# Performance work log

Hardware: AMD Instinct MI355X
Metric: run time of the kernel (lower is better)

## Reference

```python
import jax, jax.numpy as jnp
import numpy as np

HS, FF, NH = 1024, 4096, 16
HD = HS // NH
EPS = 1e-5

def _ln(x, g, b):
    m = jnp.mean(x, axis=-1, keepdims=True)
    v = jnp.mean((x - m) ** 2, axis=-1, keepdims=True)
    return (x - m) * jax.lax.rsqrt(v + EPS) * g + b

def setup_inputs() -> dict:
    key = jax.random.key(0)
    ks = jax.random.split(key, 12)
    s = 1.0 / np.sqrt(HS)
    si = 1.0 / np.sqrt(FF)
    d = {
        "hidden_states": jax.random.normal(ks[0], (2, 2048, HS), dtype=jnp.float32),
        "attention_mask": jnp.zeros((2, 1, 1, 2048), dtype=jnp.float32),
        "Wq": jax.random.uniform(ks[1], (HS, HS), minval=-s, maxval=s),
        "bq": jnp.zeros((HS,), jnp.float32),
        "Wk": jax.random.uniform(ks[2], (HS, HS), minval=-s, maxval=s),
        "bk": jnp.zeros((HS,), jnp.float32),
        "Wv": jax.random.uniform(ks[3], (HS, HS), minval=-s, maxval=s),
        "bv": jnp.zeros((HS,), jnp.float32),
        "Wo": jax.random.uniform(ks[4], (HS, HS), minval=-s, maxval=s),
        "bo": jnp.zeros((HS,), jnp.float32),
        "W1": jax.random.uniform(ks[5], (HS, FF), minval=-s, maxval=s),
        "b1": jnp.zeros((FF,), jnp.float32),
        "W2": jax.random.uniform(ks[6], (FF, HS), minval=-si, maxval=si),
        "b2": jnp.zeros((HS,), jnp.float32),
        "ln1_g": jnp.ones((HS,), jnp.float32),
        "ln1_b": jnp.zeros((HS,), jnp.float32),
        "ln2_g": jnp.ones((HS,), jnp.float32),
        "ln2_b": jnp.zeros((HS,), jnp.float32),
    }
    return d

def reference(hidden_states, attention_mask, Wq, bq, Wk, bk, Wv, bv, Wo, bo,
              W1, b1, W2, b2, ln1_g, ln1_b, ln2_g, ln2_b):
    bs, S, _ = hidden_states.shape
    x = hidden_states
    # self-attention (dropout is identity in eval)
    q = (x @ Wq + bq).reshape(bs, S, NH, HD).transpose(0, 2, 1, 3)
    k = (x @ Wk + bk).reshape(bs, S, NH, HD).transpose(0, 2, 1, 3)
    v = (x @ Wv + bv).reshape(bs, S, NH, HD).transpose(0, 2, 1, 3)
    scores = jnp.einsum("bhqd,bhkd->bhqk", q, k) / np.sqrt(HD) + attention_mask
    probs = jax.nn.softmax(scores, axis=-1)
    attn = jnp.einsum("bhqk,bhkd->bhqd", probs, v)
    attn = attn.transpose(0, 2, 1, 3).reshape(bs, S, HS)
    mha = attn @ Wo + bo
    h = _ln(x + mha, ln1_g, ln1_b)
    # FFN
    ff = jax.nn.relu(h @ W1 + b1) @ W2 + b2
    return _ln(h + ff, ln2_g, ln2_b)
```

## Files before the change

kernel.cpp:

```cpp
#include <hip/hip_runtime.h>
#include <hip/hip_bf16.h>

#define HS   1024
#define FF   4096
#define NH   16
#define HD   64
#define SEQ  2048
#define BSZ  2
#define MROWS (BSZ * SEQ)
#define EPS  1e-5f
#define QKV_STRIDE (3 * HS)

typedef float f32x4  __attribute__((ext_vector_type(4)));
typedef short bf16x8 __attribute__((ext_vector_type(8)));

#if __has_builtin(__builtin_amdgcn_exp2f)
#define EXP2(x) __builtin_amdgcn_exp2f(x)
#else
#define EXP2(x) exp2f(x)
#endif

__device__ __forceinline__ unsigned short f2bf(float x) {
  unsigned int u = __float_as_uint(x);
  u += 0x7fffu + ((u >> 16) & 1u);
  return (unsigned short)(u >> 16);
}

__device__ __forceinline__ float bf2f(unsigned short u) {
  return __uint_as_float((unsigned int)u << 16);
}

__device__ __forceinline__ unsigned int pkbf(float a, float b) {
  union { __hip_bfloat162 h; unsigned int u; } x;
  x.h = __float22bfloat162_rn(float2{a, b});
  return x.u;
}

__device__ __forceinline__ void async16(const ushort* g, ushort* lds) {
  __builtin_amdgcn_global_load_lds(
      (const __attribute__((address_space(1))) unsigned int*)g,
      (__attribute__((address_space(3))) unsigned int*)lds, 16, 0, 0);
}

template <int TBM, int TBN, bool RELU, bool OUT_BF16, bool PARTIAL>
__global__ __launch_bounds__(256) void gemm_bf16_kernel(
    const ushort* __restrict__ A, const ushort* __restrict__ Bt,
    const float* __restrict__ bias, void* __restrict__ Cout,
    int M, int N, int K, int kLen, size_t zstride)
{
  constexpr int MI = TBM / 32;
  constexpr int NJ = TBN / 32;
  __shared__ ushort As[TBM * 64];
  __shared__ ushort Bs[TBN * 64];

  const int tid = threadIdx.x;
  const int wv = tid >> 6, ln = tid & 63;

  const unsigned nxy = gridDim.x * gridDim.y;
  unsigned id = blockIdx.y * gridDim.x + blockIdx.x;
  id = (id & 7) * (nxy >> 3) + (id >> 3);
  const int bn = id % gridDim.x, bm = id / gridDim.x;

  const int lr = ln & 15;
  const int lg = ln >> 4;
  const int mrow_base = (wv >> 1) * (TBM / 2);
  const int ncol_base = (wv & 1) * (TBN / 2);

  f32x4 acc[MI][NJ];
#pragma unroll
  for (int i = 0; i < MI; ++i)
#pragma unroll
    for (int j = 0; j < NJ; ++j) acc[i][j] = (f32x4){0.f, 0.f, 0.f, 0.f};

  const int rr = ln >> 3, cc = ln & 7;
  const int kBeg = blockIdx.z * kLen, kEnd = kBeg + kLen;

  for (int k0 = kBeg; k0 < kEnd; k0 += 64) {
    __syncthreads();
#pragma unroll
    for (int t = 0; t < TBM / 32; ++t) {
      const int R = wv * (TBM / 4) + t * 8 + rr;
      const int c = cc ^ (R & 7);
      async16(A + (size_t)(bm * TBM + R) * K + k0 + c * 8,
              &As[(size_t)(wv * (TBM / 4) + t * 8) * 64]);
    }
#pragma unroll
    for (int t = 0; t < TBN / 32; ++t) {
      const int R = wv * (TBN / 4) + t * 8 + rr;
      const int c = cc ^ (R & 7);
      async16(Bt + (size_t)(bn * TBN + R) * K + k0 + c * 8,
              &Bs[(size_t)(wv * (TBN / 4) + t * 8) * 64]);
    }
    __syncthreads();

#pragma unroll
    for (int s = 0; s < 2; ++s) {
      bf16x8 a[MI], b[NJ];
#pragma unroll
      for (int i = 0; i < MI; ++i) {
        const int m = mrow_base + i * 16 + lr;
        a[i] = *(const bf16x8*)&As[(size_t)m * 64 + (((s * 4 + lg) ^ (m & 7)) * 8)];
      }
#pragma unroll
      for (int j = 0; j < NJ; ++j) {
        const int n = ncol_base + j * 16 + lr;
        b[j] = *(const bf16x8*)&Bs[(size_t)n * 64 + (((s * 4 + lg) ^ (n & 7)) * 8)];
      }
#pragma unroll
      for (int i = 0; i < MI; ++i)
#pragma unroll
        for (int j = 0; j < NJ; ++j)
          acc[i][j] = __builtin_amdgcn_mfma_f32_16x16x32_bf16(a[i], b[j], acc[i][j], 0, 0, 0);
    }
  }

  const int gm0 = bm * TBM + mrow_base;
  const int gn0 = bn * TBN + ncol_base;

  if (PARTIAL) {
    float* Cp = (float*)Cout + (size_t)blockIdx.z * zstride;
#pragma unroll
    for (int i = 0; i < MI; ++i)
#pragma unroll
      for (int r = 0; r < 4; ++r) {
        const size_t row = (size_t)(gm0 + i * 16 + lg * 4 + r);
#pragma unroll
        for (int j = 0; j < NJ; ++j)
          Cp[row * N + gn0 + j * 16 + lr] = acc[i][j][r];
      }
  } else {
    float bs4[NJ];
#pragma unroll
    for (int j = 0; j < NJ; ++j) bs4[j] = bias[gn0 + j * 16 + lr];
    float* Cf = (float*)Cout;
    ushort* Cb = (ushort*)Cout;
#pragma unroll
    for (int i = 0; i < MI; ++i) {
#pragma unroll
      for (int r = 0; r < 4; ++r) {
        const size_t row = (size_t)(gm0 + i * 16 + lg * 4 + r);
#pragma unroll
        for (int j = 0; j < NJ; ++j) {
          float val = acc[i][j][r] + bs4[j];
          if (RELU) val = fmaxf(val, 0.f);
          const size_t idx = row * N + gn0 + j * 16 + lr;
          if (OUT_BF16) Cb[idx] = f2bf(val);
          else          Cf[idx] = val;
        }
      }
    }
  }
}

__device__ __forceinline__ void transpose_tile(
    const float* __restrict__ W, ushort* __restrict__ Wt,
    int K, int N, int n0, int k0, int tid, ushort (*T)[72])
{
#pragma unroll
  for (int t = 0; t < 4; ++t) {
    const int r = t * 16 + (tid >> 4);
    const int c = (tid & 15) * 4;
    const float4 w = *(const float4*)&W[(size_t)(k0 + r) * N + n0 + c];
    T[c + 0][r] = f2bf(w.x); T[c + 1][r] = f2bf(w.y);
    T[c + 2][r] = f2bf(w.z); T[c + 3][r] = f2bf(w.w);
  }
  __syncthreads();
#pragma unroll
  for (int t = 0; t < 4; ++t) {
    const int n = t * 16 + (tid >> 4);
    const int kc = (tid & 15) * 4;
    ushort4 o;
    o.x = T[n][kc]; o.y = T[n][kc + 1]; o.z = T[n][kc + 2]; o.w = T[n][kc + 3];
    *(ushort4*)&Wt[(size_t)(n0 + n) * K + k0 + kc] = o;
  }
}

__global__ __launch_bounds__(256) void prep_kernel(
    const float* __restrict__ Wq, const float* __restrict__ Wk,
    const float* __restrict__ Wv, const float* __restrict__ Wo,
    const float* __restrict__ W1, const float* __restrict__ W2,
    const float* __restrict__ bq, const float* __restrict__ bk,
    const float* __restrict__ bv, const float* __restrict__ x,
    const float* __restrict__ mask,
    ushort* __restrict__ Wqkvt, ushort* __restrict__ Wot,
    ushort* __restrict__ W1t, ushort* __restrict__ W2t,
    float* __restrict__ bqkv, ushort* __restrict__ xb,
    float* __restrict__ maskL2)
{
  __shared__ ushort T[64][72];
  const int b = blockIdx.x, tid = threadIdx.x;
  const size_t M1 = 1024 * 1024;
  if (b < 1024) {
    const int w = b >> 8, l = b & 255;
    const int n0 = (l & 15) * 64, k0 = (l >> 4) * 64;
    const float* src = (w == 0) ? Wq : (w == 1) ? Wk : (w == 2) ? Wv : Wo;
    ushort* dst = (w < 3) ? (Wqkvt + (size_t)w * M1) : Wot;
    transpose_tile(src, dst, HS, HS, n0, k0, tid, T);
  } else if (b < 2048) {
    const int l = b - 1024;
    transpose_tile(W1, W1t, HS, FF, (l & 63) * 64, (l >> 6) * 64, tid, T);
  } else if (b < 3072) {
    const int l = b - 2048;
    transpose_tile(W2, W2t, FF, HS, (l & 15) * 64, (l >> 4) * 64, tid, T);
  } else if (b < 5120) {
    const size_t base = (size_t)(b - 3072) * 2048 + tid * 8;
    const float4 v0 = *(const float4*)&x[base];
    const float4 v1 = *(const float4*)&x[base + 4];
    ushort4 o0, o1;
    o0.x = f2bf(v0.x); o0.y = f2bf(v0.y); o0.z = f2bf(v0.z); o0.w = f2bf(v0.w);
    o1.x = f2bf(v1.x); o1.y = f2bf(v1.y); o1.z = f2bf(v1.z); o1.w = f2bf(v1.w);
    *(ushort4*)&xb[base] = o0;
    *(ushort4*)&xb[base + 4] = o1;
  } else {
#pragma unroll
    for (int t = 0; t < 12; ++t) {
      const int i = t * 256 + tid;
      bqkv[i] = (i < HS) ? bq[i] : (i < 2 * HS) ? bk[i - HS] : bv[i - 2 * HS];
    }
#pragma unroll
    for (int t = 0; t < 16; ++t) {
      const int i = t * 256 + tid;
      maskL2[i] = mask[i] * 1.44269504f;
    }
  }
}

__global__ __launch_bounds__(256) void vtrans_kernel(
    const ushort* __restrict__ vb, ushort* __restrict__ VTg, int stride)
{
  __shared__ ushort T[64][68];
  const int tid = threadIdx.x;
  const int s0 = blockIdx.x * 64;
  const int bh = blockIdx.y;
  const int b = bh >> 4, h = bh & 15;
#pragma unroll
  for (int t = 0; t < 4; ++t) {
    const int rr = t * 16 + (tid >> 4);
    const int c4 = (tid & 15) * 4;
    const ushort4 w = *(const ushort4*)&vb[(size_t)(b * SEQ + s0 + rr) * stride + h * 64 + c4];
    T[c4 + 0][rr] = w.x; T[c4 + 1][rr] = w.y;
    T[c4 + 2][rr] = w.z; T[c4 + 3][rr] = w.w;
  }
  __syncthreads();
#pragma unroll
  for (int t = 0; t < 4; ++t) {
    const int d = t * 16 + (tid >> 4);
    const int k4 = (tid & 15) * 4;
    ushort4 o;
    o.x = T[d][k4]; o.y = T[d][k4 + 1]; o.z = T[d][k4 + 2]; o.w = T[d][k4 + 3];
    *(ushort4*)&VTg[((size_t)bh * 64 + d) * SEQ + s0 + k4] = o;
  }
}

__global__ __launch_bounds__(512, 2) void attention_mfma_kernel(
    const ushort* __restrict__ Qb, const ushort* __restrict__ Kb,
    const ushort* __restrict__ VTg, const float* __restrict__ maskL2,
    ushort* __restrict__ O)
{
  __shared__ ushort smem[36864];
  float* mL = (float*)(smem + 32768);

  const int tid = threadIdx.x;
  const int wv = tid >> 6, ln = tid & 63;
  const int c = ln & 15, g = ln >> 4;

  const unsigned d0 = blockIdx.x + 8u * (blockIdx.y + 16u * blockIdx.z);
  const unsigned w0 = (d0 & 7) * 32 + (d0 >> 3);
  const int qt = w0 & 7;
  const int hh = (w0 >> 3) & 15;
  const int b  = w0 >> 7;

  const int bh = b * NH + hh;
  const size_t row0 = (size_t)b * SEQ + (size_t)qt * 256;
  const int ch = hh * HD;
  const int wq0 = wv * 32;

  bf16x8 qf[2][2];
#pragma unroll
  for (int nt = 0; nt < 2; ++nt)
#pragma unroll
    for (int s = 0; s < 2; ++s)
      qf[nt][s] = *(const bf16x8*)&Qb[(row0 + wq0 + nt * 16 + c) * QKV_STRIDE + ch + s * 32 + g * 8];

  const float* mrow = maskL2 + (size_t)b * SEQ;
  async16((const ushort*)(mrow + wv * 256 + ln * 4), (ushort*)(mL + wv * 256));

  const int rr = ln >> 3, cc = ln & 7;
  const int r4 = ln >> 4, sc = ln & 15;

  auto stage = [&](int kb, int bsel) {
    ushort* Ks  = smem + bsel * 16384;
    ushort* VTs = Ks + 8192;
    const size_t krow0 = (size_t)b * SEQ + (size_t)kb * 128;
#pragma unroll
    for (int t = 0; t < 2; ++t) {
      const int r = wv * 16 + t * 8 + rr;
      async16(Kb + (krow0 + r) * QKV_STRIDE + ch + ((cc ^ (r & 7)) * 8),
              &Ks[(size_t)(wv * 16 + t * 8) * 64]);
    }
#pragma unroll
    for (int t = 0; t < 2; ++t) {
      const int d = wv * 8 + t * 4 + r4;
      const int srcc = (sc & 8) | ((sc & 7) ^ (d & 7));
      async16(VTg + ((size_t)bh * 64 + d) * SEQ + kb * 128 + srcc * 8,
              &VTs[(size_t)(wv * 8 + t * 4) * 128]);
    }
  };

  f32x4 ao[4][2];
#pragma unroll
  for (int i = 0; i < 4; ++i) { ao[i][0] = (f32x4){0,0,0,0}; ao[i][1] = (f32x4){0,0,0,0}; }
  float l_r[2] = {0.f, 0.f};

  stage(0, 0);

  for (int kb = 0; kb < SEQ / 128; ++kb) {
    const int cur = kb & 1;
    __builtin_amdgcn_s_barrier();
    __builtin_amdgcn_sched_barrier(0);
    if (kb + 1 < SEQ / 128) {
      stage(kb + 1, cur ^ 1);
      asm volatile("s_waitcnt vmcnt(4)" ::: "memory");
    } else {
      asm volatile("s_waitcnt vmcnt(0)" ::: "memory");
    }
    __builtin_amdgcn_s_barrier();
    __builtin_amdgcn_sched_barrier(0);

    ushort* Ks  = smem + cur * 16384;
    ushort* VTs = Ks + 8192;

    f32x4 as_[8][2];
#pragma unroll
    for (int i = 0; i < 8; ++i) { as_[i][0] = (f32x4){0,0,0,0}; as_[i][1] = (f32x4){0,0,0,0}; }
    __builtin_amdgcn_s_setprio(1);
#pragma unroll
    for (int s = 0; s < 2; ++s) {
#pragma unroll
      for (int mt = 0; mt < 8; ++mt) {
        const int key = mt * 16 + c;
        const bf16x8 kf = *(const bf16x8*)&Ks[(size_t)key * 64 + (((s * 4 + g) ^ (key & 7)) * 8)];
#pragma unroll
        for (int nt = 0; nt < 2; ++nt)
          as_[mt][nt] = __builtin_amdgcn_mfma_f32_16x16x32_bf16(kf, qf[nt][s], as_[mt][nt], 0, 0, 0);
      }
    }
    __builtin_amdgcn_s_setprio(0);

#pragma unroll
    for (int mt = 0; mt < 8; ++mt) {
      const float4 mk = *(const float4*)&mL[kb * 128 + mt * 16 + g * 4];
      const float mka[4] = {mk.x, mk.y, mk.z, mk.w};
#pragma unroll
      for (int nt = 0; nt < 2; ++nt) {
#pragma unroll
        for (int r = 0; r < 4; ++r) {
          const float p = EXP2(fmaf(as_[mt][nt][r], 0.18033688f, mka[r]));
          as_[mt][nt][r] = p;
          l_r[nt] += p;
        }
      }
    }

#pragma unroll
    for (int s = 0; s < 4; ++s) {
      bf16x8 pf[2];
#pragma unroll
      for (int nt = 0; nt < 2; ++nt) {
        const unsigned A0 = pkbf(as_[2 * s][nt][0], as_[2 * s][nt][1]);
        const unsigned A1 = pkbf(as_[2 * s][nt][2], as_[2 * s][nt][3]);
        const unsigned B0 = pkbf(as_[2 * s + 1][nt][0], as_[2 * s + 1][nt][1]);
        const unsigned B1 = pkbf(as_[2 * s + 1][nt][2], as_[2 * s + 1][nt][3]);
        auto x0 = __builtin_amdgcn_permlane32_swap(A0, B0, false, false);
        auto x1 = __builtin_amdgcn_permlane32_swap(A1, B1, false, false);
        auto y0 = __builtin_amdgcn_permlane16_swap(x0[0], x0[1], false, false);
        auto y1 = __builtin_amdgcn_permlane16_swap(x1[0], x1[1], false, false);
        union { unsigned w[4]; bf16x8 v; } u;
        u.w[0] = y0[0]; u.w[1] = y1[0]; u.w[2] = y0[1]; u.w[3] = y1[1];
        pf[nt] = u.v;
      }
      __builtin_amdgcn_s_setprio(1);
#pragma unroll
      for (int mt = 0; mt < 4; ++mt) {
        const int d = mt * 16 + c;
        const int k = s * 4 + g;
        const int vslot = (k & 8) | ((k & 7) ^ (d & 7));
        const bf16x8 vf = *(const bf16x8*)&VTs[(size_t)d * 128 + vslot * 8];
#pragma unroll
        for (int nt = 0; nt < 2; ++nt)
          ao[mt][nt] = __builtin_amdgcn_mfma_f32_16x16x32_bf16(vf, pf[nt], ao[mt][nt], 0, 0, 0);
      }
      __builtin_amdgcn_s_setprio(0);
    }
  }

#pragma unroll
  for (int nt = 0; nt < 2; ++nt) {
    l_r[nt] += __shfl_xor(l_r[nt], 16, 64);
    l_r[nt] += __shfl_xor(l_r[nt], 32, 64);
  }

  __syncthreads();
  ushort* OL = smem;
#pragma unroll
  for (int nt = 0; nt < 2; ++nt) {
    const float inv = 1.f / l_r[nt];
    const int q = wq0 + nt * 16 + c;
#pragma unroll
    for (int mt = 0; mt < 4; ++mt) {
      const int d = mt * 16 + g * 4;
      uint2 w;
      w.x = pkbf(ao[mt][nt][0] * inv, ao[mt][nt][1] * inv);
      w.y = pkbf(ao[mt][nt][2] * inv, ao[mt][nt][3] * inv);
      *(uint2*)&OL[q * 72 + d] = w;
    }
  }
  __syncthreads();
#pragma unroll
  for (int it = 0; it < 4; ++it) {
    const int unit = it * 512 + tid;
    const int q = unit >> 3, sg = unit & 7;
    const uint4 w = *(const uint4*)&OL[q * 72 + sg * 8];
    *(uint4*)&O[(row0 + q) * HS + ch + sg * 8] = w;
  }
}

template <bool EMIT16>
__global__ __launch_bounds__(256) void add_ln_red_kernel(
    const float* __restrict__ P0, const float* __restrict__ P1,
    const float* __restrict__ bias, const float* __restrict__ X,
    const float* __restrict__ g, const float* __restrict__ b,
    float* __restrict__ out, ushort* __restrict__ outb)
{
  const int row = blockIdx.x;
  const int tid = threadIdx.x;
  const size_t base = (size_t)row * HS + tid * 4;
  const float4 p0 = *(const float4*)&P0[base];
  const float4 p1 = *(const float4*)&P1[base];
  const float4 bi = *(const float4*)&bias[tid * 4];
  const float4 xv = *(const float4*)&X[base];
  float4 v;
  v.x = xv.x + p0.x + p1.x + bi.x;
  v.y = xv.y + p0.y + p1.y + bi.y;
  v.z = xv.z + p0.z + p1.z + bi.z;
  v.w = xv.w + p0.w + p1.w + bi.w;
  float s1 = v.x + v.y + v.z + v.w;
  float s2 = v.x * v.x + v.y * v.y + v.z * v.z + v.w * v.w;
#pragma unroll
  for (int off = 32; off > 0; off >>= 1) {
    s1 += __shfl_down(s1, off, 64);
    s2 += __shfl_down(s2, off, 64);
  }
  __shared__ float red[8];
  __shared__ float stat[2];
  const int wid = tid >> 6;
  if ((tid & 63) == 0) { red[wid] = s1; red[4 + wid] = s2; }
  __syncthreads();
  if (tid == 0) {
    const float t1 = red[0] + red[1] + red[2] + red[3];
    const float t2 = red[4] + red[5] + red[6] + red[7];
    const float mean = t1 * (1.f / HS);
    const float var = t2 * (1.f / HS) - mean * mean;
    stat[0] = mean;
    stat[1] = rsqrtf(var + EPS);
  }
  __syncthreads();
  const float mean = stat[0], rstd = stat[1];
  const float4 gv = *(const float4*)&g[tid * 4];
  const float4 bv = *(const float4*)&b[tid * 4];
  float4 r;
  r.x = (v.x - mean) * rstd * gv.x + bv.x;
  r.y = (v.y - mean) * rstd * gv.y + bv.y;
  r.z = (v.z - mean) * rstd * gv.z + bv.z;
  r.w = (v.w - mean) * rstd * gv.w + bv.w;
  *(float4*)&out[base] = r;
  if (EMIT16) {
    ushort4 o;
    o.x = f2bf(r.x); o.y = f2bf(r.y); o.z = f2bf(r.z); o.w = f2bf(r.w);
    *(ushort4*)&outb[base] = o;
  }
}

__global__ __launch_bounds__(256) void add_ln_bf16_kernel(
    const ushort* __restrict__ Pb, const float* __restrict__ X,
    const float* __restrict__ g, const float* __restrict__ b,
    float* __restrict__ out, ushort* __restrict__ outb)
{
  const int row = blockIdx.x;
  const int tid = threadIdx.x;
  const size_t base = (size_t)row * HS + tid * 4;
  const ushort4 pb = *(const ushort4*)&Pb[base];
  const float4 xv = *(const float4*)&X[base];
  float4 v;
  v.x = xv.x + bf2f(pb.x);
  v.y = xv.y + bf2f(pb.y);
  v.z = xv.z + bf2f(pb.z);
  v.w = xv.w + bf2f(pb.w);
  float s1 = v.x + v.y + v.z + v.w;
  float s2 = v.x * v.x + v.y * v.y + v.z * v.z + v.w * v.w;
#pragma unroll
  for (int off = 32; off > 0; off >>= 1) {
    s1 += __shfl_down(s1, off, 64);
    s2 += __shfl_down(s2, off, 64);
  }
  __shared__ float red[8];
  __shared__ float stat[2];
  const int wid = tid >> 6;
  if ((tid & 63) == 0) { red[wid] = s1; red[4 + wid] = s2; }
  __syncthreads();
  if (tid == 0) {
    const float t1 = red[0] + red[1] + red[2] + red[3];
    const float t2 = red[4] + red[5] + red[6] + red[7];
    const float mean = t1 * (1.f / HS);
    const float var = t2 * (1.f / HS) - mean * mean;
    stat[0] = mean;
    stat[1] = rsqrtf(var + EPS);
  }
  __syncthreads();
  const float mean = stat[0], rstd = stat[1];
  const float4 gv = *(const float4*)&g[tid * 4];
  const float4 bv = *(const float4*)&b[tid * 4];
  float4 r;
  r.x = (v.x - mean) * rstd * gv.x + bv.x;
  r.y = (v.y - mean) * rstd * gv.y + bv.y;
  r.z = (v.z - mean) * rstd * gv.z + bv.z;
  r.w = (v.w - mean) * rstd * gv.w + bv.w;
  *(float4*)&out[base] = r;
  ushort4 o;
  o.x = f2bf(r.x); o.y = f2bf(r.y); o.z = f2bf(r.z); o.w = f2bf(r.w);
  *(ushort4*)&outb[base] = o;
}

extern "C" void kernel_launch(void* const* d_in, const int* in_sizes, int n_in,
                              void* d_out, int out_size, void* d_ws, size_t ws_size,
                              hipStream_t stream)
{
  const float* x    = (const float*)d_in[0];
  const float* mask = (const float*)d_in[1];
  const float* Wq   = (const float*)d_in[2];  const float* bq  = (const float*)d_in[3];
  const float* Wk   = (const float*)d_in[4];  const float* bk  = (const float*)d_in[5];
  const float* Wv   = (const float*)d_in[6];  const float* bv  = (const float*)d_in[7];
  const float* Wo   = (const float*)d_in[8];  const float* bo  = (const float*)d_in[9];
  const float* W1   = (const float*)d_in[10]; const float* b1  = (const float*)d_in[11];
  const float* W2   = (const float*)d_in[12]; const float* b2  = (const float*)d_in[13];
  const float* g1   = (const float*)d_in[14]; const float* be1 = (const float*)d_in[15];
  const float* g2   = (const float*)d_in[16]; const float* be2 = (const float*)d_in[17];
  float* out = (float*)d_out;

  ushort* wsu = (ushort*)d_ws;
  const size_t M1 = 1024 * 1024;

  ushort* Wqkvt = wsu;
  ushort* Wot   = wsu + 3 * M1;
  ushort* W1t   = wsu + 4 * M1;
  ushort* W2t   = wsu + 8 * M1;
  float*  bqkv  = (float*)(wsu + 12 * M1);
  float*  maskL2= (float*)(wsu + 12 * M1 + 8192);
  ushort* xb    = wsu + 13 * M1;
  ushort* qkvb  = wsu + 17 * M1;
  ushort* VTg   = wsu + 29 * M1;
  ushort* attnb = wsu + 33 * M1;
  ushort* mhab  = wsu + 13 * M1;
  float*  h     = (float*)(wsu + 29 * M1);
  ushort* hb    = wsu + 37 * M1;
  ushort* ff1o  = wsu + 13 * M1;
  float*  ff2P0 = (float*)wsu;
  float*  ff2P1 = (float*)(wsu + 39 * M1);

  const dim3 blk(256);

  prep_kernel<<<dim3(5121), blk, 0, stream>>>(
      Wq, Wk, Wv, Wo, W1, W2, bq, bk, bv, x, mask,
      Wqkvt, Wot, W1t, W2t, bqkv, xb, maskL2);

  gemm_bf16_kernel<128, 128, false, true, false><<<dim3(24, 32), blk, 0, stream>>>(
      xb, Wqkvt, bqkv, qkvb, MROWS, 3 * HS, HS, HS, 0);

  vtrans_kernel<<<dim3(SEQ / 64, BSZ * NH), blk, 0, stream>>>(qkvb + 2 * HS, VTg, QKV_STRIDE);

  attention_mfma_kernel<<<dim3(SEQ / 256, NH, BSZ), dim3(512), 0, stream>>>(
      qkvb, qkvb + HS, VTg, maskL2, attnb);

  gemm_bf16_kernel<64, 128, false, true, false><<<dim3(8, 64), blk, 0, stream>>>(
      attnb, Wot, bo, mhab, MROWS, HS, HS, HS, 0);
  add_ln_bf16_kernel<<<dim3(MROWS), blk, 0, stream>>>(
      mhab, x, g1, be1, h, hb);

  gemm_bf16_kernel<128, 128, true, true, false><<<dim3(32, 32), blk, 0, stream>>>(
      hb, W1t, b1, ff1o, MROWS, FF, HS, HS, 0);
  gemm_bf16_kernel<128, 128, false, false, true><<<dim3(8, 32, 2), blk, 0, stream>>>(
      ff1o, W2t, nullptr, ff2P0, MROWS, HS, FF, FF / 2, (size_t)(ff2P1 - ff2P0));
  add_ln_red_kernel<false><<<dim3(MROWS), blk, 0, stream>>>(
      ff2P0, ff2P1, b2, h, g2, be2, out, nullptr);
}
```

Baseline: 356.7 us.

## Add 256x256 8-wave pipelined GEMM for QKV and FFN1 projections

Adds a new bf16 GEMM kernel with 256x256 tiles, 512 threads (8 waves), double-buffered 128KB LDS with XOR swizzle, and a hand-scheduled interleaving of async global->LDS loads with MFMA quadrants using barriers and s_setprio. It replaces the 128x128 GEMM for the QKV and W1 projections to raise data reuse per tile and overlap loads with compute. The trade-off is fewer blocks (192 and 256) on a large GPU, 128KB LDS per block, and very high register pressure from 32 accumulators per lane.

```diff
diff --git a/kernel.cpp b/kernel.cpp
--- a/kernel.cpp
+++ b/kernel.cpp
@@ -40,6 +40,134 @@
   __builtin_amdgcn_global_load_lds(
       (const __attribute__((address_space(1))) unsigned int*)g,
       (__attribute__((address_space(3))) unsigned int*)lds, 16, 0, 0);
+}
+
+#define BARSB { __builtin_amdgcn_s_barrier(); __builtin_amdgcn_sched_barrier(0); }
+
+#define QUAD(kt, MH, NH)                                                      \
+  {                                                                           \
+    const ushort* As_ = &smem[(size_t)((kt) & 1) * 32768];                    \
+    const ushort* Bs_ = As_ + 16384;                                          \
+    bf16x8 af[4][2], bfr[2][2];                                               \
+    _Pragma("unroll")                                                         \
+    for (int mt = 0; mt < 4; ++mt)                                            \
+      _Pragma("unroll")                                                       \
+      for (int s = 0; s < 2; ++s) {                                           \
+        const int m = wr * 128 + (MH) * 64 + mt * 16 + lr;                    \
+        af[mt][s] = *(const bf16x8*)&As_[(size_t)m * 64 +                     \
+                                         (((s * 4 + lg) ^ (m & 7)) * 8)];     \
+      }                                                                       \
+    _Pragma("unroll")                                                         \
+    for (int nj = 0; nj < 2; ++nj)                                            \
+      _Pragma("unroll")                                                       \
+      for (int s = 0; s < 2; ++s) {                                           \
+        const int n = wc * 64 + (NH) * 32 + nj * 16 + lr;                     \
+        bfr[nj][s] = *(const bf16x8*)&Bs_[(size_t)n * 64 +                    \
+                                          (((s * 4 + lg) ^ (n & 7)) * 8)];    \
+      }                                                                       \
+    __builtin_amdgcn_s_setprio(1);                                            \
+    _Pragma("unroll")                                                         \
+    for (int s = 0; s < 2; ++s)                                               \
+      _Pragma("unroll")                                                       \
+      for (int mt = 0; mt < 4; ++mt)                                          \
+        _Pragma("unroll")                                                     \
+        for (int nj = 0; nj < 2; ++nj)                                        \
+          acc[(MH) * 4 + mt][(NH) * 2 + nj] =                                 \
+              __builtin_amdgcn_mfma_f32_16x16x32_bf16(                        \
+                  af[mt][s], bfr[nj][s], acc[(MH) * 4 + mt][(NH) * 2 + nj],   \
+                  0, 0, 0);                                                   \
+    __builtin_amdgcn_s_setprio(0);                                            \
+  }
+
+template <bool RELU>
+__global__ __launch_bounds__(512, 2) void gemm8_bf16_kernel(
+    const ushort* __restrict__ A, const ushort* __restrict__ Bt,
+    const float* __restrict__ bias, ushort* __restrict__ C,
+    int M, int N, int K)
+{
+  __shared__ ushort smem[65536];
+  const int tid = threadIdx.x;
+  const int wv = tid >> 6, ln = tid & 63;
+  const int wr = wv >> 2, wc = wv & 3;
+  const int lr = ln & 15, lg = ln >> 4;
+  const int rr = ln >> 3, cc = ln & 7;
+
+  const unsigned nxy = gridDim.x * gridDim.y;
+  unsigned id = blockIdx.y * gridDim.x + blockIdx.x;
+  id = (id & 7) * (nxy >> 3) + (id >> 3);
+  const int bn = id % gridDim.x, bm = id / gridDim.x;
+
+  f32x4 acc[8][4];
+#pragma unroll
+  for (int i = 0; i < 8; ++i)
+#pragma unroll
+    for (int j = 0; j < 4; ++j) acc[i][j] = (f32x4){0.f, 0.f, 0.f, 0.f};
+
+  auto stA = [&](int kt, int h) {
+#pragma unroll
+    for (int u = 0; u < 2; ++u) {
+      const int tt = h + u * 2;
+      const int R = tt * 64 + wv * 8 + rr;
+      async16(A + (size_t)(bm * 256 + R) * K + kt * 64 + ((cc ^ (R & 7)) * 8),
+              &smem[(size_t)(kt & 1) * 32768 + (size_t)(tt * 64 + wv * 8) * 64]);
+    }
+  };
+  auto stB = [&](int kt, int h) {
+#pragma unroll
+    for (int u = 0; u < 2; ++u) {
+      const int tt = h * 2 + u;
+      const int R = tt * 64 + wv * 8 + rr;
+      async16(Bt + (size_t)(bn * 256 + R) * K + kt * 64 + ((cc ^ (R & 7)) * 8),
+              &smem[(size_t)(kt & 1) * 32768 + 16384 + (size_t)(tt * 64 + wv * 8) * 64]);
+    }
+  };
+
+  stA(0, 0); stA(0, 1); stB(0, 0); stB(0, 1); stA(1, 0);
+
+  const int nIter = K >> 7;
+  for (int j = 0; j < nIter; ++j) {
+    const int t0 = 2 * j, t1 = t0 + 1;
+    const bool nx = (j + 1 < nIter);
+    BARSB;
+    stA(t1, 1);
+    asm volatile("s_waitcnt vmcnt(4)" ::: "memory");
+    BARSB;
+    QUAD(t0, 0, 0);
+    BARSB; stB(t1, 0); QUAD(t0, 0, 1);
+    BARSB; if (nx) stA(t0 + 2, 0); QUAD(t0, 1, 0);
+    BARSB; stB(t1, 1); QUAD(t0, 1, 1);
+    BARSB;
+    if (nx) {
+      stA(t0 + 2, 1);
+      asm volatile("s_waitcnt vmcnt(2)" ::: "memory");
+    } else {
+      asm volatile("s_waitcnt vmcnt(0)" ::: "memory");
+    }
+    BARSB;
+    QUAD(t1, 0, 0);
+    BARSB; if (nx) stB(t0 + 2, 0); QUAD(t1, 0, 1);
+    BARSB; if (nx) stB(t0 + 2, 1); QUAD(t1, 1, 0);
+    BARSB; if (nx) stA(t0 + 3, 0); QUAD(t1, 1, 1);
+  }
+
+  const int gm0 = bm * 256 + wr * 128;
+  const int gn0 = bn * 256 + wc * 64;
+  float bs4[4];
+#pragma unroll
+  for (int j = 0; j < 4; ++j) bs4[j] = bias[gn0 + j * 16 + lr];
+#pragma unroll
+  for (int i = 0; i < 8; ++i) {
+#pragma unroll
+    for (int r = 0; r < 4; ++r) {
+      const size_t row = (size_t)(gm0 + i * 16 + lg * 4 + r);
+#pragma unroll
+      for (int j = 0; j < 4; ++j) {
+        float val = acc[i][j][r] + bs4[j];
+        if (RELU) val = fmaxf(val, 0.f);
+        C[row * N + gn0 + j * 16 + lr] = f2bf(val);
+      }
+    }
+  }
 }
 
 template <int TBM, int TBN, bool RELU, bool OUT_BF16, bool PARTIAL>
@@ -573,8 +701,8 @@
       Wq, Wk, Wv, Wo, W1, W2, bq, bk, bv, x, mask,
       Wqkvt, Wot, W1t, W2t, bqkv, xb, maskL2);
 
-  gemm_bf16_kernel<128, 128, false, true, false><<<dim3(24, 32), blk, 0, stream>>>(
-      xb, Wqkvt, bqkv, qkvb, MROWS, 3 * HS, HS, HS, 0);
+  gemm8_bf16_kernel<false><<<dim3(12, 16), dim3(512), 0, stream>>>(
+      xb, Wqkvt, bqkv, qkvb, MROWS, 3 * HS, HS);
 
   vtrans_kernel<<<dim3(SEQ / 64, BSZ * NH), blk, 0, stream>>>(qkvb + 2 * HS, VTg, QKV_STRIDE);
 
@@ -586,8 +714,9 @@
   add_ln_bf16_kernel<<<dim3(MROWS), blk, 0, stream>>>(
       mhab, x, g1, be1, h, hb);
 
-  gemm_bf16_kernel<128, 128, true, true, false><<<dim3(32, 32), blk, 0, stream>>>(
-      hb, W1t, b1, ff1o, MROWS, FF, HS, HS, 0);
+  gemm8_bf16_kernel<true><<<dim3(16, 16), dim3(512), 0, stream>>>(
+      hb, W1t, b1, ff1o, MROWS, FF, HS);
+
   gemm_bf16_kernel<128, 128, false, false, true><<<dim3(8, 32, 2), blk, 0, stream>>>(
       ff1o, W2t, nullptr, ff2P0, MROWS, HS, FF, FF / 2, (size_t)(ff2P1 - ff2P0));
   add_ln_red_kernel<false><<<dim3(MROWS), blk, 0, stream>>>(
```

Result: faster. 336.0 us (-5.8%).
